# Optimization experiments

Measured on AMD Instinct MI355X. Metric: run time of the kernel, lower is better.

Reference implementation:

```python
import jax, jax.numpy as jnp
import numpy as np

A = 9
H = 384
W = 384
MIN_SIZE = 2.0
NMS_THRESH = 0.7
PRE_NMS = 6000
POST_NMS = 300


def _make_anchors():
    # anchors.generate_anchors((H, W), box_sizes): per-cell (x1, y1, w, h) boxes in
    # feature-map coordinates, one box per (anchor, y, x).
    sizes = []
    for s in (4.0, 8.0, 16.0):
        for r in (0.5, 1.0, 2.0):
            sizes.append((s * np.sqrt(r), s / np.sqrt(r)))
    ys, xs = np.meshgrid(np.arange(H, dtype=np.float32), np.arange(W, dtype=np.float32), indexing='ij')
    cx, cy = xs + 0.5, ys + 0.5
    anch = np.stack([
        np.stack([cx - w / 2, cy - h / 2, np.full_like(cx, w), np.full_like(cx, h)], axis=-1)
        for (w, h) in sizes
    ], axis=0)  # [A, H, W, 4]
    return jnp.asarray(anch, jnp.float32)


def setup_inputs() -> dict:
    key = jax.random.key(0)
    k1, k2 = jax.random.split(key)
    scores = jax.random.uniform(k1, (1, A, H, W), dtype=jnp.float32)
    bbox_deltas = jax.random.normal(k2, (1, 4 * A, H, W), dtype=jnp.float32)
    return {
        'scores': scores,
        'bbox_deltas': bbox_deltas,
        'anchor_boxes': _make_anchors(),
        'image_metadata': jnp.zeros((1, 3), jnp.float32),
    }


def _clip_boxes(boxes, length, width):
    # clip_boxes_batch: clamp everything to >=0, convert (x,y,w,h)->(x1,y1,x2,y2),
    # clip to feature-map bounds, convert back.
    b = jnp.maximum(boxes, 0.0)
    x1, y1, w, h = b[..., 0], b[..., 1], b[..., 2], b[..., 3]
    x2 = x1 + w - 1.0
    y2 = y1 + h - 1.0
    x1 = jnp.minimum(x1, length - 1.0)
    y1 = jnp.minimum(y1, width - 1.0)
    x2 = jnp.minimum(x2, length - 1.0)
    y2 = jnp.minimum(y2, width - 1.0)
    return jnp.stack([x1, y1, x2 - x1 + 1.0, y2 - y1 + 1.0], axis=-1)


def _nms(boxes, valid):
    # Faithful port of the source's sequential NMS: repeatedly pick the remaining
    # box with the largest y2, suppress boxes whose intersection / own-area >= thresh.
    x1, y1, w, h = boxes[:, 0], boxes[:, 1], boxes[:, 2], boxes[:, 3]
    x2 = x1 + w - 1.0
    y2 = y1 + h - 1.0
    areas = w * h
    NEG = jnp.float32(-1e30)

    def cond(st):
        v, keep, cnt = st
        return (cnt < POST_NMS) & jnp.any(v)

    def body(st):
        v, keep, cnt = st
        ind = jnp.argmax(jnp.where(v, y2, NEG))
        xx1 = jnp.maximum(x1, x1[ind])
        yy1 = jnp.maximum(y1, y1[ind])
        xx2 = jnp.minimum(x2, x2[ind])
        yy2 = jnp.minimum(y2, y2[ind])
        inter = jnp.maximum(xx2 - xx1 + 1.0, 0.0) * jnp.maximum(yy2 - yy1 + 1.0, 0.0)
        ratio = inter / areas  # intersection over each candidate's own area (as in source)
        nv = v & (ratio < NMS_THRESH)
        nv = nv.at[ind].set(False)
        return nv, keep.at[cnt].set(ind.astype(jnp.int32)), cnt + 1

    keep0 = jnp.full((POST_NMS,), -1, jnp.int32)
    _, keep, cnt = jax.lax.while_loop(cond, body, (valid, keep0, jnp.int32(0)))
    return keep, cnt


def reference(scores, bbox_deltas, anchor_boxes, image_metadata):
    B = 1
    _, _, Hh, Ww = scores.shape
    # two contiguous .view()s compose to a single reshape
    deltas = bbox_deltas.reshape(B, A, Hh, Ww, 4)
    boxes = anchor_boxes[None] + deltas               # [1, A, H, W, 4]
    clipped = _clip_boxes(boxes, float(Hh), float(Ww))
    keep = (clipped[..., 2] >= MIN_SIZE) & (clipped[..., 3] >= MIN_SIZE)

    N = A * Hh * Ww
    boxes_f = clipped.reshape(N, 4)
    scores_f = scores.reshape(N)
    masked = jnp.where(keep.reshape(N), scores_f, jnp.float32(-jnp.inf))

    # descending score sort, PRE_NMS_TOP_N truncation
    order = jnp.argsort(-masked)[:PRE_NMS]
    props = boxes_f[order]                            # [PRE_NMS, 4]
    sc = masked[order]
    valid = jnp.isfinite(sc)

    keep_idx, cnt = _nms(props, valid)
    sel = props[jnp.maximum(keep_idx, 0)]             # [POST_NMS, 4]
    slot_valid = jnp.arange(POST_NMS) < cnt
    out = jnp.where(slot_valid[:, None], sel, 0.0)[None]  # [1, POST_NMS, 4]
    return out
```

## Files before the change

kernel.cpp:

```cpp
#include <hip/hip_runtime.h>
#include <stdint.h>

#define NN 1327104
#define NQ 331776
#define NB 1296
#define PRE_NMS_ 6000
#define POST_NMS_ 300
#define LB_CAP 16384
#define NPAD 6144
#define NWORD 96
#define KB 16
#define MATB 192
#define NREP 8


static __device__ __forceinline__ uint32_t score_key(float s) {
  uint32_t b = __float_as_uint(s);
  uint32_t u = b ^ (((int32_t)b < 0) ? 0xFFFFFFFFu : 0x80000000u);
  return ~u;
}

static __device__ __forceinline__ uint32_t f2s(float v) {
  uint32_t b = __float_as_uint(v);
  return b ^ (((int32_t)b < 0) ? 0xFFFFFFFFu : 0x80000000u);
}

static __device__ __forceinline__ void compute_box(float4 an, float4 de,
    float& x1, float& y1, float& wc, float& hc, bool& keep) {
  float bx = fmaxf(an.x + de.x, 0.0f);
  float by = fmaxf(an.y + de.y, 0.0f);
  float bw = fmaxf(an.z + de.z, 0.0f);
  float bh = fmaxf(an.w + de.w, 0.0f);
  float x2 = bx + bw - 1.0f;
  float y2 = by + bh - 1.0f;
  x1 = fminf(bx, 383.0f);
  y1 = fminf(by, 383.0f);
  x2 = fminf(x2, 383.0f);
  y2 = fminf(y2, 383.0f);
  wc = x2 - x1 + 1.0f;
  hc = y2 - y1 + 1.0f;
  keep = (wc >= 2.0f) && (hc >= 2.0f);
}

static __device__ __forceinline__ uint32_t kb18_of(float s) {
  return (uint32_t)(s * 262144.0f);
}

static __device__ __forceinline__ uint32_t wscan(uint32_t v, int l) {
  #pragma unroll
  for (int off = 1; off < 64; off <<= 1) {
    uint32_t u = __shfl_up(v, off);
    if (l >= off) v += u;
  }
  return v;
}

static __device__ __forceinline__ void pick1_f(const uint32_t* __restrict__ h1r,
                                               uint32_t& selR8, uint32_t& base1) {
  int l = threadIdx.x & 63;
  uint32_t a0 = 0, a1 = 0, a2 = 0, a3 = 0, a4 = 0;
  #pragma unroll
  for (int r = 0; r < NREP; ++r) {
    const uint32_t* h1 = h1r + r * 320;
    a0 += h1[l*5]; a1 += h1[l*5+1]; a2 += h1[l*5+2]; a3 += h1[l*5+3]; a4 += h1[l*5+4];
  }
  uint32_t c0 = a0, c1 = c0+a1, c2 = c1+a2, c3 = c2+a3, c4 = c3+a4;
  uint32_t inc = wscan(c4, l);
  uint32_t excl = inc - c4;
  bool hit = (excl < PRE_NMS_) && (inc >= PRE_NMS_);
  unsigned long long hb = __ballot(hit);
  int hl = __ffsll(hb) - 1;
  uint32_t k, cb;
  if      (excl + c0 >= PRE_NMS_) { k = 0; cb = 0;  }
  else if (excl + c1 >= PRE_NMS_) { k = 1; cb = c0; }
  else if (excl + c2 >= PRE_NMS_) { k = 2; cb = c1; }
  else if (excl + c3 >= PRE_NMS_) { k = 3; cb = c2; }
  else                            { k = 4; cb = c3; }
  selR8 = __shfl(l*5u + k, hl);
  base1 = __shfl(excl + cb, hl);
}

static __device__ __forceinline__ void pickT_lds(const uint32_t* __restrict__ h2,
                                                 uint32_t T,
                                                 uint32_t& sel10, uint32_t& base) {
  int l = threadIdx.x & 63;
  uint32_t h[16];
  #pragma unroll
  for (int k = 0; k < 16; ++k) h[k] = h2[l*16 + k];
  uint32_t cum[16]; cum[0] = h[0];
  #pragma unroll
  for (int k = 1; k < 16; ++k) cum[k] = cum[k-1] + h[k];
  uint32_t inc = wscan(cum[15], l);
  uint32_t excl = inc - cum[15];
  bool hit = (excl < T) && (inc >= T);
  unsigned long long hb = __ballot(hit);
  int hl = __ffsll(hb) - 1;
  uint32_t k = 15, cb = cum[14];
  #pragma unroll
  for (int kk = 15; kk >= 0; --kk)
    if (excl + cum[kk] >= T) { k = (uint32_t)kk; cb = kk ? cum[kk-1] : 0u; }
  sel10 = __shfl(l*16u + k, hl);
  base  = __shfl(excl + cb, hl);
}

static __device__ __forceinline__ void emit_item(uint32_t pos, uint32_t d, uint32_t idx,
    const float4* __restrict__ deltas, const float4* __restrict__ anchors,
    uint64_t* __restrict__ keyhi, uint32_t* __restrict__ keylo,
    float4* __restrict__ box4u) {
  float x1, y1, wc, hc; bool keep;
  compute_box(anchors[idx], deltas[idx], x1, y1, wc, hc, keep);
  float y2 = y1 + hc - 1.0f;
  keyhi[pos] = ((uint64_t)f2s(y2) << 32) | (uint32_t)(~d);
  keylo[pos] = ~idx;
  box4u[pos] = make_float4(x1, y1, wc, hc);
}

__global__ __launch_bounds__(256) void k_hA(const float* __restrict__ scores,
                                            const float4* __restrict__ deltas,
                                            const float4* __restrict__ anchors,
                                            uint32_t* __restrict__ darr,
                                            uint32_t* __restrict__ hist1r,
                                            uint32_t* __restrict__ zctr) {
  __shared__ uint32_t lh[320];
  int t = threadIdx.x;
  for (int j = t; j < 320; j += 256) lh[j] = 0;
  __syncthreads();
  int base = blockIdx.x * 256 + t;
  #pragma unroll
  for (int it = 0; it < 4; ++it) {
    int i = base + it * NQ;
    float x1, y1, wc, hc; bool keep;
    compute_box(anchors[i], deltas[i], x1, y1, wc, hc, keep);
    float s = scores[i];
    uint32_t d = keep ? score_key(s) : 0xFF800000u;
    darr[i] = d;
    uint32_t r8 = keep ? (255u - (kb18_of(s) >> 10)) : 256u;
    atomicAdd(&lh[r8], 1u);
  }
  __syncthreads();
  uint32_t* hdst = hist1r + (blockIdx.x & (NREP - 1)) * 320;
  for (int j = t; j < 320; j += 256) {
    uint32_t c = lh[j];
    if (c) atomicAdd(&hdst[j], c);
  }
  if (blockIdx.x == 0) for (int j = t; j < 320; j += 256) zctr[j] = 0;
}

__global__ __launch_bounds__(256) void k_gather(const uint4* __restrict__ dv,
                                                const uint32_t* __restrict__ hist1r,
                                                uint32_t* __restrict__ ctr,
                                                uint64_t* __restrict__ Lb,
                                                uint64_t* __restrict__ keyhi,
                                                uint32_t* __restrict__ keylo,
                                                float4* __restrict__ box4u,
                                                const float4* __restrict__ deltas,
                                                const float4* __restrict__ anchors) {
  __shared__ uint64_t stA[1024];
  __shared__ uint64_t stB[1024];
  __shared__ uint32_t nA, nB, baseA, baseB, s_sel8;
  int t = threadIdx.x;
  if (t < 64) {
    uint32_t sel8, base1;
    pick1_f(hist1r, sel8, base1);
    if (t == 0) { s_sel8 = sel8; nA = 0; nB = 0; }
  }
  __syncthreads();
  uint32_t selR8 = s_sel8;

  int g = blockIdx.x * 256 + t;
  uint4 v = dv[g];
  uint32_t arr[4] = {v.x, v.y, v.z, v.w};
  #pragma unroll
  for (int k = 0; k < 4; ++k) {
    uint32_t d = arr[k];
    uint32_t idx = (uint32_t)(g * 4 + k);
    uint32_t r8 = (d <= 0x7FFFFFFFu)
                ? (255u - (kb18_of(__uint_as_float(0x7FFFFFFFu - d)) >> 10)) : 256u;
    if (r8 < selR8) {
      uint32_t p = atomicAdd(&nA, 1u);
      stA[p] = ((uint64_t)d << 32) | idx;
    } else if (r8 == selR8) {
      uint32_t q = atomicAdd(&nB, 1u);
      stB[q] = ((uint64_t)d << 32) | idx;
    }
  }
  __syncthreads();
  if (t == 0) {
    baseA = nA ? atomicAdd(&ctr[0], nA)  : 0u;
    baseB = nB ? atomicAdd(&ctr[32], nB) : 0u;
  }
  __syncthreads();
  uint32_t mA = nA, mB = nB, bA = baseA, bB = baseB;
  for (uint32_t j = t; j < mA; j += 256) {
    uint64_t kj = stA[j];
    uint32_t p = bA + j;
    if (p < PRE_NMS_)
      emit_item(p, (uint32_t)(kj >> 32), (uint32_t)kj, deltas, anchors,
                keyhi, keylo, box4u);
  }
  for (uint32_t j = t; j < mB; j += 256) {
    uint32_t q = bB + j;
    if (q < LB_CAP) Lb[q] = stB[j];
  }
}

__global__ __launch_bounds__(256) void k_finish(const uint32_t* __restrict__ ctr,
                                                const uint64_t* __restrict__ Lb,
                                                uint64_t* __restrict__ keyhi,
                                                uint32_t* __restrict__ keylo,
                                                float4* __restrict__ box4u,
                                                const float4* __restrict__ deltas,
                                                const float4* __restrict__ anchors) {
  __shared__ uint32_t lh2[1024];
  __shared__ uint64_t bnd[256];
  __shared__ uint32_t bcnt, lcnt, s_sel10, s_base;
  int t = threadIdx.x;
  for (int j = t; j < 1024; j += 256) lh2[j] = 0;
  if (t == 0) { bcnt = 0; lcnt = 0; }
  __syncthreads();

  uint32_t C1 = ctr[0]; if (C1 > PRE_NMS_) C1 = PRE_NMS_;
  uint32_t Cb = ctr[32]; if (Cb > LB_CAP) Cb = LB_CAP;
  uint32_t T = PRE_NMS_ - C1;

  for (uint32_t j = t; j < Cb; j += 256) {
    uint32_t d = (uint32_t)(Lb[j] >> 32);
    uint32_t r10 = (d <= 0x7FFFFFFFu)
                 ? (1023u - (kb18_of(__uint_as_float(0x7FFFFFFFu - d)) & 1023u)) : 0u;
    atomicAdd(&lh2[r10], 1u);
  }
  __syncthreads();
  if (t < 64) {
    uint32_t sel10 = 0xFFFFFFFFu, b2 = 0;
    if (T > 0) pickT_lds(lh2, T, sel10, b2);
    if (t == 0) { s_sel10 = sel10; s_base = b2; }
  }
  __syncthreads();
  uint32_t sel10 = s_sel10, C2base = s_base;

  for (uint32_t j = t; j < Cb; j += 256) {
    uint64_t kj = Lb[j];
    uint32_t d = (uint32_t)(kj >> 32), idx = (uint32_t)kj;
    uint32_t r10 = (d <= 0x7FFFFFFFu)
                 ? (1023u - (kb18_of(__uint_as_float(0x7FFFFFFFu - d)) & 1023u)) : 0u;
    if (r10 < sel10) {
      uint32_t p = C1 + atomicAdd(&lcnt, 1u);
      if (p < PRE_NMS_) emit_item(p, d, idx, deltas, anchors, keyhi, keylo, box4u);
    } else if (r10 == sel10) {
      uint32_t q = atomicAdd(&bcnt, 1u);
      if (q < 256) bnd[q] = kj;
    }
  }
  __syncthreads();
  uint32_t B = (bcnt < 256u) ? bcnt : 256u;
  uint32_t T2 = (T > C2base) ? (T - C2base) : 0u;
  for (uint32_t j = t; j < B; j += 256) {
    uint64_t kj = bnd[j];
    uint32_t r = 0;
    for (uint32_t k = 0; k < B; ++k) r += (bnd[k] < kj) ? 1u : 0u;
    if (r < T2)
      emit_item(C1 + C2base + r, (uint32_t)(kj >> 32), (uint32_t)kj,
                deltas, anchors, keyhi, keylo, box4u);
  }
  for (int j = PRE_NMS_ + t; j < NPAD; j += 256) {
    keyhi[j] = 0;
    keylo[j] = (uint32_t)(NPAD - j);
    box4u[j] = make_float4(0.f, 0.f, 0.f, 0.f);
  }
}

__global__ __launch_bounds__(512) void k_rank(const uint64_t* __restrict__ keyhi,
                                              const uint32_t* __restrict__ keylo,
                                              uint32_t* __restrict__ rank2d) {
  __shared__ uint64_t shi[768];
  __shared__ uint32_t slo[768];
  int t = threadIdx.x;
  int ib = blockIdx.x >> 3, c = blockIdx.x & 7, base = c * 768;
  for (int j = t; j < 768; j += 512) { shi[j] = keyhi[base + j]; slo[j] = keylo[base + j]; }
  __syncthreads();
  int i = ib * 256 + (t >> 1);
  int h = t & 1;
  uint64_t hi = keyhi[i]; uint32_t lo = keylo[i];
  uint32_t cnt = 0;
  int j0 = h * 384;
  for (int j = j0; j < j0 + 384; ++j) {
    uint64_t hj = shi[j]; uint32_t lj = slo[j];
    cnt += ((hj > hi) || (hj == hi && lj > lo)) ? 1u : 0u;
  }
  rank2d[i * 16 + c * 2 + h] = cnt;
}

__global__ __launch_bounds__(512) void k_matsc(const uint64_t* __restrict__ keyhi,
                                               const uint32_t* __restrict__ rank2d,
                                               const float4* __restrict__ box4u,
                                               float4* __restrict__ sobox,
                                               unsigned long long* __restrict__ valid,
                                               uint64_t* __restrict__ M) {
  __shared__ float4 sb[NPAD];
  __shared__ float  sa[NPAD];
  int t = threadIdx.x;
  int b = blockIdx.x;
  for (int i = t; i < NPAD; i += 512) {
    const uint4* rp = (const uint4*)(rank2d + (size_t)i * 16);
    uint4 r0 = rp[0], r1 = rp[1], r2 = rp[2], r3 = rp[3];
    uint32_t r = r0.x+r0.y+r0.z+r0.w + r1.x+r1.y+r1.z+r1.w
               + r2.x+r2.y+r2.z+r2.w + r3.x+r3.y+r3.z+r3.w;
    float4 bx = box4u[i];
    float x2 = bx.x + bx.z - 1.0f;
    float y2 = bx.y + bx.w - 1.0f;
    sb[r] = make_float4(bx.x, bx.y, x2, y2);
    sa[r] = bx.z * bx.w;
    if (b == 0) {
      sobox[r] = bx;
      uint32_t d = ~(uint32_t)(keyhi[i] & 0xFFFFFFFFu);
      if (d < 0xFF800000u)
        atomicOr(&valid[r >> 6], 1ull << (r & 63));
    }
  }
  __syncthreads();
  int wid = t >> 6, l = t & 63;
  #pragma unroll
  for (int rr = 0; rr < 4; ++rr) {
    int r = b * 32 + wid * 4 + rr;
    float4 rb = sb[r];
    for (int w = 0; w < NWORD; ++w) {
      int j = w * 64 + l;
      float4 cb = sb[j];
      float ca = sa[j];
      float xx1 = fmaxf(cb.x, rb.x), yy1 = fmaxf(cb.y, rb.y);
      float xx2 = fminf(cb.z, rb.z), yy2 = fminf(cb.w, rb.w);
      float iw = fmaxf(xx2 - xx1 + 1.0f, 0.0f);
      float ih = fmaxf(yy2 - yy1 + 1.0f, 0.0f);
      float ratio = (iw * ih) / ca;
      unsigned long long mm = __ballot(!(ratio < 0.7f));
      if (l == 0) M[(size_t)r * NWORD + w] = mm;
    }
  }
}

#define FOR16(F) F(0) F(1) F(2) F(3) F(4) F(5) F(6) F(7) \
                 F(8) F(9) F(10) F(11) F(12) F(13) F(14) F(15)

__global__ __launch_bounds__(64) void k_seq(const unsigned long long* __restrict__ valid,
                                            const uint64_t* __restrict__ M,
                                            const float4* __restrict__ sobox,
                                            float* __restrict__ out) {
  __shared__ int cslot[KB];
  int l = threadIdx.x;
  unsigned long long v0 = valid[l];
  unsigned long long v1 = (l < 32) ? valid[64 + l] : 0ull;
  uint32_t cnt = 0;

  for (;;) {
    uint32_t n0 = (uint32_t)__popcll(v0);
    uint32_t inc0 = wscan(n0, l);
    uint32_t T0 = __shfl(inc0, 63);
    uint32_t ex0 = inc0 - n0;
    uint32_t n1 = (uint32_t)__popcll(v1);
    uint32_t inc1 = wscan(n1, l);
    uint32_t T1 = __shfl(inc1, 63);
    uint32_t ex1 = T0 + inc1 - n1;
    uint32_t TV = T0 + T1;
    if (cnt >= POST_NMS_ || TV == 0) break;
    uint32_t m = (TV < KB) ? TV : KB;

    __syncthreads();
    if (l < KB) cslot[l] = 0;
    __syncthreads();
    if (ex0 < KB) {
      unsigned long long w = v0; uint32_t r = ex0;
      while (w && r < KB) { int b = __ffsll(w) - 1; cslot[r] = l * 64 + b; ++r; w &= w - 1; }
    }
    if (ex1 < KB && v1) {
      unsigned long long w = v1; uint32_t r = ex1;
      while (w && r < KB) { int b = __ffsll(w) - 1; cslot[r] = (64 + l) * 64 + b; ++r; w &= w - 1; }
    }
    __syncthreads();

#define ROWDECL(k) uint64_t rm0_##k = 0, rm1_##k = 0;
    FOR16(ROWDECL)
#undef ROWDECL
#define ROWLOAD(k) if (k < (int)m) { const uint64_t* p = M + (size_t)cslot[k] * NWORD; \
                     rm0_##k = p[l]; rm1_##k = (l < 32) ? p[64 + l] : 0ull; }
    FOR16(ROWLOAD)
#undef ROWLOAD
    float4 obox = make_float4(0.f, 0.f, 0.f, 0.f);
    if (l < KB) obox = sobox[cslot[l]];

    uint32_t cj = (l < KB) ? (uint32_t)cslot[l] : 0u;
    uint32_t wj = cj >> 6, bj = cj & 63;
    int srcA = (int)(wj & 63), srcB = (int)(wj & 31);
    uint32_t srow[KB];
#define SROW(k) { uint64_t a = __shfl((unsigned long long)rm0_##k, srcA); \
                  uint64_t b = __shfl((unsigned long long)rm1_##k, srcB); \
                  uint64_t sel = (wj < 64) ? a : b; \
                  uint32_t bit = (l < KB && k < (int)m) ? (uint32_t)((sel >> bj) & 1) : 0u; \
                  srow[k] = (uint32_t)(__ballot(bit) & 0xFFFFull); }
    FOR16(SROW)
#undef SROW

    uint32_t cnt0 = cnt;
    uint32_t wm = 0, supp = 0;
    #pragma unroll
    for (int k = 0; k < KB; ++k) {
      if (k < (int)m && cnt < POST_NMS_ && !((supp >> k) & 1)) {
        wm |= 1u << k; ++cnt; supp |= srow[k];
      }
    }

    if (l < KB && ((wm >> l) & 1)) {
      uint32_t pos = cnt0 + (uint32_t)__popc(wm & ((1u << l) - 1));
      *(float4*)(out + (size_t)pos * 4) = obox;
    }

    uint64_t comb0 = 0, comb1 = 0;
#define COMB(k) if ((wm >> k) & 1) { comb0 |= rm0_##k; comb1 |= rm1_##k; }
    FOR16(COMB)
#undef COMB
    v0 &= ~comb0; v1 &= ~comb1;
  }

  for (int j = l; j < (int)(POST_NMS_ - cnt) * 4; j += 64) out[cnt * 4 + j] = 0.0f;
}

extern "C" void kernel_launch(void* const* d_in, const int* in_sizes, int n_in,
                              void* d_out, int out_size, void* d_ws, size_t ws_size,
                              hipStream_t stream) {
  const float*  scores  = (const float*)d_in[0];
  const float4* deltas  = (const float4*)d_in[1];
  const float4* anchors = (const float4*)d_in[2];
  float* out = (float*)d_out;

  uint8_t* w8 = (uint8_t*)d_ws;
  uint32_t* darr  = (uint32_t*)w8;
  uint64_t* M     = (uint64_t*)w8;
  float4*   sobox = (float4*)(w8 + 4841472);
  uint64_t* keyhi  = (uint64_t*)(w8 + 5308416);
  uint32_t* keylo  = (uint32_t*)(w8 + 5357568);
  float4*   box4u  = (float4*)  (w8 + 5382144);
  uint32_t* rank2d = (uint32_t*)(w8 + 5480448);
  uint32_t* hist1r = (uint32_t*)(w8 + 5873664);
  uint32_t* ctr    = (uint32_t*)(w8 + 5883904);
  unsigned long long* valid = (unsigned long long*)(w8 + 5884160);
  uint64_t* Lb     = (uint64_t*)(w8 + 5885184);

  const uint4* dv = (const uint4*)darr;

  hipMemsetAsync(hist1r, 0, 10240, stream);

  k_hA    <<<NB, 256, 0, stream>>>(scores, deltas, anchors, darr, hist1r, ctr);
  k_gather<<<NB, 256, 0, stream>>>(dv, hist1r, ctr, Lb, keyhi, keylo, box4u,
                                   deltas, anchors);
  k_finish<<<1, 256, 0, stream>>>(ctr, Lb, keyhi, keylo, box4u, deltas, anchors);
  k_rank  <<<MATB, 512, 0, stream>>>(keyhi, keylo, rank2d);
  k_matsc <<<MATB, 512, 0, stream>>>(keyhi, rank2d, box4u, sobox, valid, M);
  k_seq   <<<1, 64, 0, stream>>>(valid, M, sobox, out);
}
```

Before: 255.4 us.

## Prefetch suppression matrix into cache with helper waves in sequential NMS kernel

Launches the sequential NMS kernel with 1024 threads. The 15 extra waves stream the suppression matrix and sorted boxes through an XOR reduction, which pulls them into cache ahead of the single working wave. The working wave raises its priority and replaces __syncthreads with sched barriers, since it is the only wave touching the shared slots. It also skips the second-half popcount scan when the first half already supplies enough candidates. The prefetch waves compete for memory bandwidth and CU issue slots, and dropping the barriers leans on single-wave LDS ordering.

```diff
diff --git a/kernel.cpp b/kernel.cpp
--- a/kernel.cpp
+++ b/kernel.cpp
@@ -341,32 +341,54 @@
 #define FOR16(F) F(0) F(1) F(2) F(3) F(4) F(5) F(6) F(7) \
                  F(8) F(9) F(10) F(11) F(12) F(13) F(14) F(15)
 
-__global__ __launch_bounds__(64) void k_seq(const unsigned long long* __restrict__ valid,
-                                            const uint64_t* __restrict__ M,
-                                            const float4* __restrict__ sobox,
-                                            float* __restrict__ out) {
+__global__ __launch_bounds__(1024) void k_seq(const unsigned long long* __restrict__ valid,
+                                              const uint64_t* __restrict__ M,
+                                              const float4* __restrict__ sobox,
+                                              float* __restrict__ out) {
   __shared__ int cslot[KB];
-  int l = threadIdx.x;
+  int t = threadIdx.x;
+  if (t >= 64) {
+    const uint4* p = (const uint4*)M;
+    uint4 acc = make_uint4(0, 0, 0, 0);
+    for (int j = t - 64; j < 4096 * 48; j += 960) {
+      uint4 v = p[j];
+      acc.x ^= v.x; acc.y ^= v.y; acc.z ^= v.z; acc.w ^= v.w;
+    }
+    const uint4* q = (const uint4*)sobox;
+    for (int j = t - 64; j < NPAD; j += 960) {
+      uint4 v = q[j];
+      acc.x ^= v.x; acc.y ^= v.y; acc.z ^= v.z; acc.w ^= v.w;
+    }
+    asm volatile("" :: "v"(acc.x), "v"(acc.y), "v"(acc.z), "v"(acc.w));
+    return;
+  }
+  __builtin_amdgcn_s_setprio(1);
+  int l = t;
   unsigned long long v0 = valid[l];
   unsigned long long v1 = (l < 32) ? valid[64 + l] : 0ull;
   uint32_t cnt = 0;
 
   for (;;) {
+    if (cnt >= POST_NMS_) break;
     uint32_t n0 = (uint32_t)__popcll(v0);
     uint32_t inc0 = wscan(n0, l);
     uint32_t T0 = __shfl(inc0, 63);
     uint32_t ex0 = inc0 - n0;
-    uint32_t n1 = (uint32_t)__popcll(v1);
-    uint32_t inc1 = wscan(n1, l);
-    uint32_t T1 = __shfl(inc1, 63);
-    uint32_t ex1 = T0 + inc1 - n1;
-    uint32_t TV = T0 + T1;
-    if (cnt >= POST_NMS_ || TV == 0) break;
-    uint32_t m = (TV < KB) ? TV : KB;
-
-    __syncthreads();
+    uint32_t m, ex1 = KB;
+    if (T0 < KB) {
+      uint32_t n1 = (uint32_t)__popcll(v1);
+      uint32_t inc1 = wscan(n1, l);
+      uint32_t T1 = __shfl(inc1, 63);
+      uint32_t TV = T0 + T1;
+      if (TV == 0) break;
+      m = (TV < KB) ? TV : KB;
+      ex1 = T0 + inc1 - n1;
+    } else {
+      m = KB;
+    }
+
     if (l < KB) cslot[l] = 0;
-    __syncthreads();
+    __builtin_amdgcn_sched_barrier(0);
     if (ex0 < KB) {
       unsigned long long w = v0; uint32_t r = ex0;
       while (w && r < KB) { int b = __ffsll(w) - 1; cslot[r] = l * 64 + b; ++r; w &= w - 1; }
@@ -375,7 +397,7 @@
       unsigned long long w = v1; uint32_t r = ex1;
       while (w && r < KB) { int b = __ffsll(w) - 1; cslot[r] = (64 + l) * 64 + b; ++r; w &= w - 1; }
     }
-    __syncthreads();
+    __builtin_amdgcn_sched_barrier(0);
 
 #define ROWDECL(k) uint64_t rm0_##k = 0, rm1_##k = 0;
     FOR16(ROWDECL)
@@ -419,6 +441,7 @@
 #undef COMB
     v0 &= ~comb0; v1 &= ~comb1;
   }
+  __builtin_amdgcn_s_setprio(0);
 
   for (int j = l; j < (int)(POST_NMS_ - cnt) * 4; j += 64) out[cnt * 4 + j] = 0.0f;
 }
@@ -454,5 +477,5 @@
   k_finish<<<1, 256, 0, stream>>>(ctr, Lb, keyhi, keylo, box4u, deltas, anchors);
   k_rank  <<<MATB, 512, 0, stream>>>(keyhi, keylo, rank2d);
   k_matsc <<<MATB, 512, 0, stream>>>(keyhi, rank2d, box4u, sobox, valid, M);
-  k_seq   <<<1, 64, 0, stream>>>(valid, M, sobox, out);
-}
+  k_seq   <<<1, 1024, 0, stream>>>(valid, M, sobox, out);
+}
```

After: 261.6 us. 1.02x slower.
